# Kernel optimization log

Hardware: AMD Instinct MI355X
Metric: run time of the kernel (lower is better)

Reference implementation:

```python
import jax, jax.numpy as jnp
import numpy as np

B, N, E, D = 1, 50000, 800000, 128


def _mlp(x, w1, b1, w2, b2, w3, b3):
    # MLP(in, hidden, out, l=2): Linear+ReLU, Linear+ReLU, Linear
    h = jax.nn.relu(x @ w1 + b1)
    h = jax.nn.relu(h @ w2 + b2)
    return h @ w3 + b3


def _glorot(key, shape):
    fan_in, fan_out = shape[0], shape[1]
    lim = np.sqrt(6.0 / (fan_in + fan_out)).astype(np.float32)
    return jax.random.uniform(key, shape, jnp.float32, -lim, lim)


def setup_inputs() -> dict:
    key = jax.random.key(0)
    ks = jax.random.split(key, 16)
    inp = {
        "nodes": jax.random.normal(ks[0], (B, N, D), jnp.float32),
        "senders": jax.random.randint(ks[1], (E,), 0, N, jnp.int32),
        "receivers": jax.random.randint(ks[2], (E,), 0, N, jnp.int32),
        # message MLP params: 2D -> D -> D -> D
        "mw1": _glorot(ks[3], (2 * D, D)), "mb1": jnp.zeros((D,), jnp.float32),
        "mw2": _glorot(ks[4], (D, D)),     "mb2": jnp.zeros((D,), jnp.float32),
        "mw3": _glorot(ks[5], (D, D)),     "mb3": jnp.zeros((D,), jnp.float32),
        # node MLP params: 2D -> D -> D -> D
        "nw1": _glorot(ks[6], (2 * D, D)), "nb1": jnp.zeros((D,), jnp.float32),
        "nw2": _glorot(ks[7], (D, D)),     "nb2": jnp.zeros((D,), jnp.float32),
        "nw3": _glorot(ks[8], (D, D)),     "nb3": jnp.zeros((D,), jnp.float32),
    }
    return inp


def reference(nodes, senders, receivers,
              mw1, mb1, mw2, mb2, mw3, mb3,
              nw1, nb1, nw2, nb2, nw3, nb3):
    # gather endpoint features: [B, E, 2D]
    edge_in = jnp.concatenate((nodes[:, receivers], nodes[:, senders]), axis=-1)
    messages = _mlp(edge_in, mw1, mb1, mw2, mb2, mw3, mb3)  # [B, E, D]
    # scatter-add messages into receiver inbox: [B, N, D]
    inbox = jnp.zeros_like(nodes).at[:, receivers].add(messages)
    node_in = jnp.concatenate((nodes, inbox), axis=-1)  # [B, N, 2D]
    return nodes + _mlp(node_in, nw1, nb1, nw2, nb2, nw3, nb3)
```

## Files before the change

kernel.cpp:

```cpp
#include <hip/hip_runtime.h>
#include <hip/hip_bf16.h>
#include <stdint.h>

typedef __bf16 bf16;
typedef bf16 bf16x8 __attribute__((ext_vector_type(8)));
typedef float f32x4 __attribute__((ext_vector_type(4)));

#define N_NODES 50000
#define FEAT 128
#define NB_SCAN ((N_NODES + 1023) / 1024)

static constexpr size_t UV_BYTES    = (size_t)N_NODES * 256 * 2;
static constexpr size_t INBOX_BYTES = (size_t)N_NODES * FEAT * 4;

#define WUV_OFF 0
#define WM2_OFF 32768
#define WM3_OFF 49152
#define WN1_OFF 65536
#define WN2_OFF 98304
#define WN3_OFF 114688
#define W_TOTAL 131072
static constexpr size_t W_BYTES = (size_t)W_TOTAL * 2;

__device__ __forceinline__ bf16x8 cvt_f32x8_bf16(const float* __restrict__ p) {
  float4 f0 = *(const float4*)p;
  float4 f1 = *(const float4*)(p + 4);
  bf16x8 t;
  t[0] = (bf16)f0.x; t[1] = (bf16)f0.y; t[2] = (bf16)f0.z; t[3] = (bf16)f0.w;
  t[4] = (bf16)f1.x; t[5] = (bf16)f1.y; t[6] = (bf16)f1.z; t[7] = (bf16)f1.w;
  return t;
}

__global__ void prep_weights_kernel(const float* __restrict__ mw1, const float* __restrict__ mw2,
                                    const float* __restrict__ mw3, const float* __restrict__ nw1,
                                    const float* __restrict__ nw2, const float* __restrict__ nw3,
                                    bf16* __restrict__ w) {
  int i = blockIdx.x * blockDim.x + threadIdx.x;
  if (i >= W_TOTAL) return;
  float v;
  if (i < WM2_OFF) {
    int c = i >> 7, k = i & 127;
    v = (c < 128) ? mw1[k * 128 + c] : mw1[(128 + k) * 128 + (c - 128)];
  } else if (i < WM3_OFF) {
    int j = i - WM2_OFF; int c = j >> 7, k = j & 127;
    v = mw2[k * 128 + c];
  } else if (i < WN1_OFF) {
    int j = i - WM3_OFF; int c = j >> 7, k = j & 127;
    v = mw3[k * 128 + c];
  } else if (i < WN2_OFF) {
    int j = i - WN1_OFF; int c = j >> 8, k = j & 255;
    v = nw1[k * 128 + c];
  } else if (i < WN3_OFF) {
    int j = i - WN2_OFF; int c = j >> 7, k = j & 127;
    v = nw2[k * 128 + c];
  } else {
    int j = i - WN3_OFF; int c = j >> 7, k = j & 127;
    v = nw3[k * 128 + c];
  }
  w[i] = (bf16)v;
}

__global__ void hist_kernel(const int* __restrict__ receivers, int* __restrict__ cnt, int E) {
  int i = blockIdx.x * blockDim.x + threadIdx.x;
  if (i < E) atomicAdd(&cnt[receivers[i]], 1);
}

__global__ __launch_bounds__(1024) void scan1_kernel(const int* __restrict__ cnt,
                                                     int* __restrict__ offs,
                                                     int* __restrict__ bsum) {
  __shared__ int s[1024];
  const int tid = threadIdx.x;
  const int g = blockIdx.x * 1024 + tid;
  int x = (g < N_NODES) ? cnt[g] : 0;
  s[tid] = x;
  __syncthreads();
  for (int off = 1; off < 1024; off <<= 1) {
    int v = (tid >= off) ? s[tid - off] : 0;
    __syncthreads();
    s[tid] += v;
    __syncthreads();
  }
  if (g < N_NODES) offs[g] = s[tid] - x;
  if (tid == 1023) bsum[blockIdx.x] = s[tid];
}

__global__ void scan2_kernel(int* __restrict__ bsum) {
  __shared__ int s[64];
  const int tid = threadIdx.x;
  int x = (tid < NB_SCAN) ? bsum[tid] : 0;
  s[tid] = x;
  __syncthreads();
  for (int off = 1; off < 64; off <<= 1) {
    int v = (tid >= off) ? s[tid - off] : 0;
    __syncthreads();
    s[tid] += v;
    __syncthreads();
  }
  if (tid < NB_SCAN) bsum[tid] = s[tid] - x;
}

__global__ __launch_bounds__(1024) void scan3_kernel(int* __restrict__ offs,
                                                     const int* __restrict__ bsum, int E) {
  const int tid = threadIdx.x;
  const int g = blockIdx.x * 1024 + tid;
  if (g < N_NODES) offs[g] += bsum[blockIdx.x];
  if (blockIdx.x == 0 && tid == 0) offs[N_NODES] = E;
}

__global__ void pos_kernel(const int* __restrict__ receivers, const int* __restrict__ offs,
                           int* __restrict__ cur, int* __restrict__ pos, int E) {
  int i = blockIdx.x * blockDim.x + threadIdx.x;
  if (i < E) {
    int r = receivers[i];
    pos[i] = offs[r] + atomicAdd(&cur[r], 1);
  }
}

__global__ __launch_bounds__(512) void uv_gemm_kernel(const float* __restrict__ nodes,
                                                      const bf16* __restrict__ wuvt,
                                                      const float* __restrict__ mb1,
                                                      bf16* __restrict__ uv) {
  const int tid = threadIdx.x;
  const int lane = tid & 63, wid = tid >> 6;
  const int wm = wid >> 2, wn = wid & 3;
  const int rBase = blockIdx.x * 128 + wm * 64;
  const int cBase = wn * 64;
  const int l15 = lane & 15, ka = (lane >> 4) * 8, rj = (lane >> 4) * 4;

  f32x4 acc[4][4];
#pragma unroll
  for (int mi = 0; mi < 4; ++mi)
#pragma unroll
    for (int ni = 0; ni < 4; ++ni) acc[mi][ni] = (f32x4){0.f, 0.f, 0.f, 0.f};

#pragma unroll
  for (int kk = 0; kk < 4; ++kk) {
    const int k0 = kk * 32 + ka;
    bf16x8 a[4], b[4];
#pragma unroll
    for (int mi = 0; mi < 4; ++mi) {
      int r = rBase + mi * 16 + l15;
      if (r > N_NODES - 1) r = N_NODES - 1;
      a[mi] = cvt_f32x8_bf16(nodes + (size_t)r * FEAT + k0);
    }
#pragma unroll
    for (int ni = 0; ni < 4; ++ni) {
      int c = cBase + ni * 16 + l15;
      b[ni] = *(const bf16x8*)(wuvt + (size_t)c * 128 + k0);
    }
#pragma unroll
    for (int mi = 0; mi < 4; ++mi)
#pragma unroll
      for (int ni = 0; ni < 4; ++ni)
        acc[mi][ni] = __builtin_amdgcn_mfma_f32_16x16x32_bf16(a[mi], b[ni], acc[mi][ni], 0, 0, 0);
  }
#pragma unroll
  for (int mi = 0; mi < 4; ++mi)
#pragma unroll
    for (int ni = 0; ni < 4; ++ni) {
      int c = cBase + ni * 16 + l15;
      float bias = (c < FEAT) ? mb1[c] : 0.f;
#pragma unroll
      for (int j = 0; j < 4; ++j) {
        int r = rBase + mi * 16 + rj + j;
        if (r < N_NODES) uv[(size_t)r * 256 + c] = (bf16)(acc[mi][ni][j] + bias);
      }
    }
}

#define EB 128
template <bool SORT>
__global__ __launch_bounds__(256, 3) void edge_kernel(const bf16* __restrict__ uv,
                                                      const int* __restrict__ senders,
                                                      const int* __restrict__ receivers,
                                                      const int* __restrict__ pos,
                                                      const bf16* __restrict__ wm2t,
                                                      const bf16* __restrict__ wm3t,
                                                      const float* __restrict__ mb2,
                                                      const float* __restrict__ mb3,
                                                      bf16* __restrict__ msg,
                                                      float* __restrict__ inbox, int E) {
  __shared__ int rIds[EB];
  __shared__ int sIds[EB];
  __shared__ int pIds[EB];
  __shared__ bf16 hbuf[4][32 * 128];

  const int tid = threadIdx.x;
  const int e0 = blockIdx.x * EB;
  const int rMax = (E - e0 < EB) ? (E - e0) : EB;

  if (tid < EB) {
    int e = e0 + tid; if (e >= E) e = E - 1;
    rIds[tid] = receivers[e];
    if (SORT) pIds[tid] = pos[e];
  } else {
    int t = tid - EB;
    int e = e0 + t; if (e >= E) e = E - 1;
    sIds[t] = senders[e];
  }
  __syncthreads();

  const int lane = tid & 63, wid = tid >> 6;
  const int l15 = lane & 15, ka = (lane >> 4) * 8, rj = (lane >> 4) * 4;
  const int rW = wid * 32;
  bf16* hw = hbuf[wid];

  bf16x8 afr[2][4];
#pragma unroll
  for (int mi = 0; mi < 2; ++mi) {
    int row = rW + mi * 16 + l15;
    int recv = rIds[row], send = sIds[row];
    const bf16* up = uv + (size_t)recv * 256;
    const bf16* vp = uv + (size_t)send * 256 + 128;
#pragma unroll
    for (int kk = 0; kk < 4; ++kk) {
      int k0 = kk * 32 + ka;
      bf16x8 u8 = *(const bf16x8*)(up + k0);
      bf16x8 v8 = *(const bf16x8*)(vp + k0);
      bf16x8 h;
#pragma unroll
      for (int t = 0; t < 8; ++t) {
        float x = (float)u8[t] + (float)v8[t];
        h[t] = (bf16)(x > 0.f ? x : 0.f);
      }
      afr[mi][kk] = h;
    }
  }

  f32x4 acc[2][8];
#pragma unroll
  for (int mi = 0; mi < 2; ++mi)
#pragma unroll
    for (int ni = 0; ni < 8; ++ni) acc[mi][ni] = (f32x4){0.f, 0.f, 0.f, 0.f};
#pragma unroll
  for (int kk = 0; kk < 4; ++kk) {
    const int k0 = kk * 32 + ka;
    bf16x8 b[8];
#pragma unroll
    for (int ni = 0; ni < 8; ++ni) {
      int c = ni * 16 + l15;
      b[ni] = *(const bf16x8*)(wm2t + (size_t)c * 128 + k0);
    }
#pragma unroll
    for (int mi = 0; mi < 2; ++mi)
#pragma unroll
      for (int ni = 0; ni < 8; ++ni)
        acc[mi][ni] = __builtin_amdgcn_mfma_f32_16x16x32_bf16(afr[mi][kk], b[ni], acc[mi][ni], 0, 0, 0);
  }

#pragma unroll
  for (int mi = 0; mi < 2; ++mi)
#pragma unroll
    for (int ni = 0; ni < 8; ++ni) {
      int c = ni * 16 + l15;
      float bias = mb2[c];
#pragma unroll
      for (int j = 0; j < 4; ++j) {
        int row = mi * 16 + rj + j;
        float v = acc[mi][ni][j] + bias;
        v = v > 0.f ? v : 0.f;
        int byte = row * 256 + ((c * 2) ^ ((row & 7) << 4));
        *(bf16*)((char*)hw + byte) = (bf16)v;
      }
    }
  asm volatile("s_waitcnt lgkmcnt(0)" ::: "memory");
  __builtin_amdgcn_sched_barrier(0);

  bf16x8 a3[2][4];
#pragma unroll
  for (int mi = 0; mi < 2; ++mi) {
    int row = mi * 16 + l15;
#pragma unroll
    for (int kk = 0; kk < 4; ++kk) {
      int k0 = kk * 32 + ka;
      int byte = row * 256 + ((k0 * 2) ^ ((row & 7) << 4));
      a3[mi][kk] = *(const bf16x8*)((const char*)hw + byte);
    }
  }
  f32x4 acc3[2][8];
#pragma unroll
  for (int mi = 0; mi < 2; ++mi)
#pragma unroll
    for (int ni = 0; ni < 8; ++ni) acc3[mi][ni] = (f32x4){0.f, 0.f, 0.f, 0.f};
#pragma unroll
  for (int kk = 0; kk < 4; ++kk) {
    const int k0 = kk * 32 + ka;
    bf16x8 b[8];
#pragma unroll
    for (int ni = 0; ni < 8; ++ni) {
      int c = ni * 16 + l15;
      b[ni] = *(const bf16x8*)(wm3t + (size_t)c * 128 + k0);
    }
#pragma unroll
    for (int mi = 0; mi < 2; ++mi)
#pragma unroll
      for (int ni = 0; ni < 8; ++ni)
        acc3[mi][ni] = __builtin_amdgcn_mfma_f32_16x16x32_bf16(a3[mi][kk], b[ni], acc3[mi][ni], 0, 0, 0);
  }

  if (SORT) {
    asm volatile("s_waitcnt lgkmcnt(0)" ::: "memory");
    __builtin_amdgcn_sched_barrier(0);
#pragma unroll
    for (int mi = 0; mi < 2; ++mi)
#pragma unroll
      for (int ni = 0; ni < 8; ++ni) {
        int c = ni * 16 + l15;
        float bias = mb3[c];
#pragma unroll
        for (int j = 0; j < 4; ++j) {
          int row = mi * 16 + rj + j;
          int byte = row * 256 + ((c * 2) ^ ((row & 7) << 4));
          *(bf16*)((char*)hw + byte) = (bf16)(acc3[mi][ni][j] + bias);
        }
      }
    asm volatile("s_waitcnt lgkmcnt(0)" ::: "memory");
    __builtin_amdgcn_sched_barrier(0);
#pragma unroll
    for (int it = 0; it < 8; ++it) {
      int idx = it * 64 + lane;
      int row = idx >> 4, ch = idx & 15;
      int byte = row * 256 + ((ch * 16) ^ ((row & 7) << 4));
      bf16x8 m = *(const bf16x8*)((const char*)hw + byte);
      int grow = rW + row;
      if (grow < rMax)
        *(bf16x8*)(msg + (size_t)pIds[grow] * FEAT + ch * 8) = m;
    }
  } else {
#pragma unroll
    for (int mi = 0; mi < 2; ++mi)
#pragma unroll
      for (int ni = 0; ni < 8; ++ni) {
        int c = ni * 16 + l15;
        float bias = mb3[c];
#pragma unroll
        for (int j = 0; j < 4; ++j) {
          int row = rW + mi * 16 + rj + j;
          if (row < rMax)
            unsafeAtomicAdd(inbox + (size_t)rIds[row] * FEAT + c, acc3[mi][ni][j] + bias);
        }
      }
  }
}

__global__ __launch_bounds__(256) void reduce_kernel(const bf16* __restrict__ msg,
                                                     const int* __restrict__ offs,
                                                     float* __restrict__ inbox) {
  const int tid = threadIdx.x;
  const int n = blockIdx.x * 64 + (tid >> 2);
  if (n >= N_NODES) return;
  const int sub = tid & 3;
  const int beg = offs[n], end = offs[n + 1];

  float acc[4][8];
#pragma unroll
  for (int q = 0; q < 4; ++q)
#pragma unroll
    for (int t = 0; t < 8; ++t) acc[q][t] = 0.f;

  for (int j = beg; j < end; ++j) {
    const bf16* row = msg + (size_t)j * FEAT + sub * 32;
#pragma unroll
    for (int q = 0; q < 4; ++q) {
      bf16x8 m = *(const bf16x8*)(row + q * 8);
#pragma unroll
      for (int t = 0; t < 8; ++t) acc[q][t] += (float)m[t];
    }
  }
  float* dst = inbox + (size_t)n * FEAT + sub * 32;
#pragma unroll
  for (int q = 0; q < 4; ++q) {
    float4 v0 = {acc[q][0], acc[q][1], acc[q][2], acc[q][3]};
    float4 v1 = {acc[q][4], acc[q][5], acc[q][6], acc[q][7]};
    *(float4*)(dst + q * 8) = v0;
    *(float4*)(dst + q * 8 + 4) = v1;
  }
}

__global__ __launch_bounds__(512) void node_kernel(const float* __restrict__ nodes,
                                                   const float* __restrict__ inbox,
                                                   const bf16* __restrict__ wn1t,
                                                   const bf16* __restrict__ wn2t,
                                                   const bf16* __restrict__ wn3t,
                                                   const float* __restrict__ nb1,
                                                   const float* __restrict__ nb2,
                                                   const float* __restrict__ nb3,
                                                   float* __restrict__ out) {
  __shared__ bf16 h1[256 * 128];
  __shared__ bf16 h2[256 * 128];
  const int tid = threadIdx.x;
  const int lane = tid & 63, wid = tid >> 6;
  const int wm = wid >> 1, wn = wid & 1;
  const int rBase = wm * 64, cBase = wn * 64;
  const int l15 = lane & 15, ka = (lane >> 4) * 8, rj = (lane >> 4) * 4;
  const int nBase = blockIdx.x * 256;

  f32x4 acc[4][4];
#pragma unroll
  for (int mi = 0; mi < 4; ++mi)
#pragma unroll
    for (int ni = 0; ni < 4; ++ni) acc[mi][ni] = (f32x4){0.f, 0.f, 0.f, 0.f};
#pragma unroll
  for (int kk = 0; kk < 8; ++kk) {
    const int k0 = kk * 32 + ka;
    bf16x8 a[4], b[4];
#pragma unroll
    for (int mi = 0; mi < 4; ++mi) {
      int n = nBase + rBase + mi * 16 + l15;
      if (n > N_NODES - 1) n = N_NODES - 1;
      const float* src = (kk < 4) ? (nodes + (size_t)n * FEAT + k0)
                                  : (inbox + (size_t)n * FEAT + (k0 - 128));
      a[mi] = cvt_f32x8_bf16(src);
    }
#pragma unroll
    for (int ni = 0; ni < 4; ++ni) {
      int c = cBase + ni * 16 + l15;
      b[ni] = *(const bf16x8*)(wn1t + (size_t)c * 256 + k0);
    }
#pragma unroll
    for (int mi = 0; mi < 4; ++mi)
#pragma unroll
      for (int ni = 0; ni < 4; ++ni)
        acc[mi][ni] = __builtin_amdgcn_mfma_f32_16x16x32_bf16(a[mi], b[ni], acc[mi][ni], 0, 0, 0);
  }
#pragma unroll
  for (int mi = 0; mi < 4; ++mi)
#pragma unroll
    for (int ni = 0; ni < 4; ++ni) {
      int c = cBase + ni * 16 + l15;
      float bias = nb1[c];
#pragma unroll
      for (int j = 0; j < 4; ++j) {
        int r = rBase + mi * 16 + rj + j;
        float v = acc[mi][ni][j] + bias;
        v = v > 0.f ? v : 0.f;
        int byte = r * 256 + ((c * 2) ^ ((r & 7) << 4));
        *(bf16*)((char*)h1 + byte) = (bf16)v;
      }
    }
  __syncthreads();

#pragma unroll
  for (int mi = 0; mi < 4; ++mi)
#pragma unroll
    for (int ni = 0; ni < 4; ++ni) acc[mi][ni] = (f32x4){0.f, 0.f, 0.f, 0.f};
#pragma unroll
  for (int kk = 0; kk < 4; ++kk) {
    const int k0 = kk * 32 + ka;
    bf16x8 a[4], b[4];
#pragma unroll
    for (int mi = 0; mi < 4; ++mi) {
      int r = rBase + mi * 16 + l15;
      int byte = r * 256 + ((k0 * 2) ^ ((r & 7) << 4));
      a[mi] = *(const bf16x8*)((const char*)h1 + byte);
    }
#pragma unroll
    for (int ni = 0; ni < 4; ++ni) {
      int c = cBase + ni * 16 + l15;
      b[ni] = *(const bf16x8*)(wn2t + (size_t)c * 128 + k0);
    }
#pragma unroll
    for (int mi = 0; mi < 4; ++mi)
#pragma unroll
      for (int ni = 0; ni < 4; ++ni)
        acc[mi][ni] = __builtin_amdgcn_mfma_f32_16x16x32_bf16(a[mi], b[ni], acc[mi][ni], 0, 0, 0);
  }
#pragma unroll
  for (int mi = 0; mi < 4; ++mi)
#pragma unroll
    for (int ni = 0; ni < 4; ++ni) {
      int c = cBase + ni * 16 + l15;
      float bias = nb2[c];
#pragma unroll
      for (int j = 0; j < 4; ++j) {
        int r = rBase + mi * 16 + rj + j;
        float v = acc[mi][ni][j] + bias;
        v = v > 0.f ? v : 0.f;
        int byte = r * 256 + ((c * 2) ^ ((r & 7) << 4));
        *(bf16*)((char*)h2 + byte) = (bf16)v;
      }
    }
  __syncthreads();

#pragma unroll
  for (int mi = 0; mi < 4; ++mi)
#pragma unroll
    for (int ni = 0; ni < 4; ++ni) acc[mi][ni] = (f32x4){0.f, 0.f, 0.f, 0.f};
#pragma unroll
  for (int kk = 0; kk < 4; ++kk) {
    const int k0 = kk * 32 + ka;
    bf16x8 a[4], b[4];
#pragma unroll
    for (int mi = 0; mi < 4; ++mi) {
      int r = rBase + mi * 16 + l15;
      int byte = r * 256 + ((k0 * 2) ^ ((r & 7) << 4));
      a[mi] = *(const bf16x8*)((const char*)h2 + byte);
    }
#pragma unroll
    for (int ni = 0; ni < 4; ++ni) {
      int c = cBase + ni * 16 + l15;
      b[ni] = *(const bf16x8*)(wn3t + (size_t)c * 128 + k0);
    }
#pragma unroll
    for (int mi = 0; mi < 4; ++mi)
#pragma unroll
      for (int ni = 0; ni < 4; ++ni)
        acc[mi][ni] = __builtin_amdgcn_mfma_f32_16x16x32_bf16(a[mi], b[ni], acc[mi][ni], 0, 0, 0);
  }
#pragma unroll
  for (int mi = 0; mi < 4; ++mi)
#pragma unroll
    for (int ni = 0; ni < 4; ++ni) {
      int c = cBase + ni * 16 + l15;
      float bias = nb3[c];
#pragma unroll
      for (int j = 0; j < 4; ++j) {
        int r = rBase + mi * 16 + rj + j;
        int n = nBase + r;
        if (n < N_NODES)
          out[(size_t)n * FEAT + c] = nodes[(size_t)n * FEAT + c] + acc[mi][ni][j] + bias;
      }
    }
}

extern "C" void kernel_launch(void* const* d_in, const int* in_sizes, int n_in,
                              void* d_out, int out_size, void* d_ws, size_t ws_size,
                              hipStream_t stream) {
  const float* nodes = (const float*)d_in[0];
  const int* senders = (const int*)d_in[1];
  const int* receivers = (const int*)d_in[2];
  const float* mw1 = (const float*)d_in[3];
  const float* mb1 = (const float*)d_in[4];
  const float* mw2 = (const float*)d_in[5];
  const float* mb2 = (const float*)d_in[6];
  const float* mw3 = (const float*)d_in[7];
  const float* mb3 = (const float*)d_in[8];
  const float* nw1 = (const float*)d_in[9];
  const float* nb1 = (const float*)d_in[10];
  const float* nw2 = (const float*)d_in[11];
  const float* nb2 = (const float*)d_in[12];
  const float* nw3 = (const float*)d_in[13];
  const float* nb3 = (const float*)d_in[14];
  float* out = (float*)d_out;
  const int E = in_sizes[1];

  char* ws = (char*)d_ws;
  bf16* uv = (bf16*)ws;
  bf16* w = (bf16*)(ws + UV_BYTES);
  char* p = ws + UV_BYTES + W_BYTES;
  float* inbox = (float*)p; p += INBOX_BYTES;

  int* offs = (int*)p; p += ((size_t)(N_NODES + 1) * 4 + 255) & ~255ull;
  int* cnt = (int*)p;  p += ((size_t)N_NODES * 4 + 255) & ~255ull;
  int* cur = (int*)p;  p += ((size_t)N_NODES * 4 + 255) & ~255ull;
  int* pos = (int*)p;  p += ((size_t)E * 4 + 255) & ~255ull;
  bf16* msg = (bf16*)p; p += (size_t)E * FEAT * 2;
  const bool sortPath = ((size_t)(p - ws) <= ws_size);

  prep_weights_kernel<<<(W_TOTAL + 255) / 256, 256, 0, stream>>>(mw1, mw2, mw3, nw1, nw2, nw3, w);
  uv_gemm_kernel<<<(N_NODES + 127) / 128, 512, 0, stream>>>(nodes, w + WUV_OFF, mb1, uv);

  if (sortPath) {
    hipMemsetAsync(cnt, 0, (size_t)N_NODES * 4, stream);
    hipMemsetAsync(cur, 0, (size_t)N_NODES * 4, stream);
    hist_kernel<<<(E + 255) / 256, 256, 0, stream>>>(receivers, cnt, E);
    scan1_kernel<<<NB_SCAN, 1024, 0, stream>>>(cnt, offs, pos);
    scan2_kernel<<<1, 64, 0, stream>>>(pos);
    scan3_kernel<<<NB_SCAN, 1024, 0, stream>>>(offs, pos, E);
    pos_kernel<<<(E + 255) / 256, 256, 0, stream>>>(receivers, offs, cur, pos, E);
    edge_kernel<true><<<(E + EB - 1) / EB, 256, 0, stream>>>(uv, senders, receivers, pos,
                                                             w + WM2_OFF, w + WM3_OFF, mb2, mb3,
                                                             msg, inbox, E);
    reduce_kernel<<<(N_NODES + 63) / 64, 256, 0, stream>>>(msg, offs, inbox);
  } else {
    hipMemsetAsync(inbox, 0, INBOX_BYTES, stream);
    edge_kernel<false><<<(E + EB - 1) / EB, 256, 0, stream>>>(uv, senders, receivers, nullptr,
                                                              w + WM2_OFF, w + WM3_OFF, mb2, mb3,
                                                              nullptr, inbox, E);
  }
  node_kernel<<<(N_NODES + 255) / 256, 512, 0, stream>>>(nodes, inbox, w + WN1_OFF, w + WN2_OFF,
                                                         w + WN3_OFF, nb1, nb2, nb3, out);
}
```

Measured before the change: 501.7 us.

## Sort edges by receiver and segment-reduce messages in-block before atomics

Edges are now permuted into receiver-sorted order by scattering sender and receiver ids, so the edge kernel processes them in sorted order. Each warp transposes its message tile through LDS and accumulates runs of equal receivers in registers, issuing one atomic per run per column pair. This removes the per-edge bf16 message buffer write and the separate reduce kernel, trading them for atomics that are far fewer than per-edge ones. Gather locality on uv changes because sender access becomes more random while receiver access becomes sequential.

```diff
diff --git a/kernel.cpp b/kernel.cpp
--- a/kernel.cpp
+++ b/kernel.cpp
@@ -107,12 +107,16 @@
   if (blockIdx.x == 0 && tid == 0) offs[N_NODES] = E;
 }
 
-__global__ void pos_kernel(const int* __restrict__ receivers, const int* __restrict__ offs,
-                           int* __restrict__ cur, int* __restrict__ pos, int E) {
+__global__ void scatter_ids_kernel(const int* __restrict__ senders,
+                                   const int* __restrict__ receivers,
+                                   const int* __restrict__ offs, int* __restrict__ cur,
+                                   int* __restrict__ sSend, int* __restrict__ sRecv, int E) {
   int i = blockIdx.x * blockDim.x + threadIdx.x;
   if (i < E) {
     int r = receivers[i];
-    pos[i] = offs[r] + atomicAdd(&cur[r], 1);
+    int slot = offs[r] + atomicAdd(&cur[r], 1);
+    sSend[slot] = senders[i];
+    sRecv[slot] = r;
   }
 }
 
@@ -169,20 +173,16 @@
 }
 
 #define EB 128
-template <bool SORT>
 __global__ __launch_bounds__(256, 3) void edge_kernel(const bf16* __restrict__ uv,
-                                                      const int* __restrict__ senders,
-                                                      const int* __restrict__ receivers,
-                                                      const int* __restrict__ pos,
+                                                      const int* __restrict__ sSend,
+                                                      const int* __restrict__ sRecv,
                                                       const bf16* __restrict__ wm2t,
                                                       const bf16* __restrict__ wm3t,
                                                       const float* __restrict__ mb2,
                                                       const float* __restrict__ mb3,
-                                                      bf16* __restrict__ msg,
                                                       float* __restrict__ inbox, int E) {
   __shared__ int rIds[EB];
   __shared__ int sIds[EB];
-  __shared__ int pIds[EB];
   __shared__ bf16 hbuf[4][32 * 128];
 
   const int tid = threadIdx.x;
@@ -191,12 +191,11 @@
 
   if (tid < EB) {
     int e = e0 + tid; if (e >= E) e = E - 1;
-    rIds[tid] = receivers[e];
-    if (SORT) pIds[tid] = pos[e];
+    rIds[tid] = sRecv[e];
   } else {
     int t = tid - EB;
     int e = e0 + t; if (e >= E) e = E - 1;
-    sIds[t] = senders[e];
+    sIds[t] = sSend[e];
   }
   __syncthreads();
 
@@ -298,82 +297,46 @@
         acc3[mi][ni] = __builtin_amdgcn_mfma_f32_16x16x32_bf16(a3[mi][kk], b[ni], acc3[mi][ni], 0, 0, 0);
   }
 
-  if (SORT) {
-    asm volatile("s_waitcnt lgkmcnt(0)" ::: "memory");
-    __builtin_amdgcn_sched_barrier(0);
-#pragma unroll
-    for (int mi = 0; mi < 2; ++mi)
-#pragma unroll
-      for (int ni = 0; ni < 8; ++ni) {
-        int c = ni * 16 + l15;
-        float bias = mb3[c];
-#pragma unroll
-        for (int j = 0; j < 4; ++j) {
-          int row = mi * 16 + rj + j;
-          int byte = row * 256 + ((c * 2) ^ ((row & 7) << 4));
-          *(bf16*)((char*)hw + byte) = (bf16)(acc3[mi][ni][j] + bias);
-        }
-      }
-    asm volatile("s_waitcnt lgkmcnt(0)" ::: "memory");
-    __builtin_amdgcn_sched_barrier(0);
-#pragma unroll
-    for (int it = 0; it < 8; ++it) {
-      int idx = it * 64 + lane;
-      int row = idx >> 4, ch = idx & 15;
-      int byte = row * 256 + ((ch * 16) ^ ((row & 7) << 4));
-      bf16x8 m = *(const bf16x8*)((const char*)hw + byte);
-      int grow = rW + row;
-      if (grow < rMax)
-        *(bf16x8*)(msg + (size_t)pIds[grow] * FEAT + ch * 8) = m;
-    }
-  } else {
-#pragma unroll
-    for (int mi = 0; mi < 2; ++mi)
-#pragma unroll
-      for (int ni = 0; ni < 8; ++ni) {
-        int c = ni * 16 + l15;
-        float bias = mb3[c];
-#pragma unroll
-        for (int j = 0; j < 4; ++j) {
-          int row = rW + mi * 16 + rj + j;
-          if (row < rMax)
-            unsafeAtomicAdd(inbox + (size_t)rIds[row] * FEAT + c, acc3[mi][ni][j] + bias);
-        }
-      }
-  }
-}
-
-__global__ __launch_bounds__(256) void reduce_kernel(const bf16* __restrict__ msg,
-                                                     const int* __restrict__ offs,
-                                                     float* __restrict__ inbox) {
-  const int tid = threadIdx.x;
-  const int n = blockIdx.x * 64 + (tid >> 2);
-  if (n >= N_NODES) return;
-  const int sub = tid & 3;
-  const int beg = offs[n], end = offs[n + 1];
-
-  float acc[4][8];
-#pragma unroll
-  for (int q = 0; q < 4; ++q)
-#pragma unroll
-    for (int t = 0; t < 8; ++t) acc[q][t] = 0.f;
-
-  for (int j = beg; j < end; ++j) {
-    const bf16* row = msg + (size_t)j * FEAT + sub * 32;
-#pragma unroll
-    for (int q = 0; q < 4; ++q) {
-      bf16x8 m = *(const bf16x8*)(row + q * 8);
-#pragma unroll
-      for (int t = 0; t < 8; ++t) acc[q][t] += (float)m[t];
-    }
-  }
-  float* dst = inbox + (size_t)n * FEAT + sub * 32;
-#pragma unroll
-  for (int q = 0; q < 4; ++q) {
-    float4 v0 = {acc[q][0], acc[q][1], acc[q][2], acc[q][3]};
-    float4 v1 = {acc[q][4], acc[q][5], acc[q][6], acc[q][7]};
-    *(float4*)(dst + q * 8) = v0;
-    *(float4*)(dst + q * 8 + 4) = v1;
+  asm volatile("s_waitcnt lgkmcnt(0)" ::: "memory");
+  __builtin_amdgcn_sched_barrier(0);
+#pragma unroll
+  for (int mi = 0; mi < 2; ++mi)
+#pragma unroll
+    for (int ni = 0; ni < 8; ++ni) {
+      int c = ni * 16 + l15;
+      float bias = mb3[c];
+#pragma unroll
+      for (int j = 0; j < 4; ++j) {
+        int row = mi * 16 + rj + j;
+        int byte = row * 256 + ((c * 2) ^ ((row & 7) << 4));
+        *(bf16*)((char*)hw + byte) = (bf16)(acc3[mi][ni][j] + bias);
+      }
+    }
+  asm volatile("s_waitcnt lgkmcnt(0)" ::: "memory");
+  __builtin_amdgcn_sched_barrier(0);
+
+  uint32_t pr[32];
+#pragma unroll
+  for (int r = 0; r < 32; ++r) {
+    int byte = r * 256 + ((4 * lane) ^ ((r & 7) << 4));
+    pr[r] = *(const uint32_t*)((const char*)hw + byte);
+  }
+  const int cb = 2 * lane;
+  float s0 = 0.f, s1 = 0.f;
+#pragma unroll
+  for (int r = 0; r < 32; ++r) {
+    int grow = rW + r;
+    if (grow >= rMax) break;
+    s0 += __uint_as_float(pr[r] << 16);
+    s1 += __uint_as_float(pr[r] & 0xffff0000u);
+    int recv = rIds[grow];
+    bool flush = (r == 31) || (grow + 1 >= rMax) || (rIds[grow + 1] != recv);
+    if (flush) {
+      float* dst = inbox + (size_t)recv * FEAT + cb;
+      unsafeAtomicAdd(dst, s0);
+      unsafeAtomicAdd(dst + 1, s1);
+      s0 = 0.f; s1 = 0.f;
+    }
   }
 }
 
@@ -549,35 +512,26 @@
   bf16* w = (bf16*)(ws + UV_BYTES);
   char* p = ws + UV_BYTES + W_BYTES;
   float* inbox = (float*)p; p += INBOX_BYTES;
-
   int* offs = (int*)p; p += ((size_t)(N_NODES + 1) * 4 + 255) & ~255ull;
   int* cnt = (int*)p;  p += ((size_t)N_NODES * 4 + 255) & ~255ull;
   int* cur = (int*)p;  p += ((size_t)N_NODES * 4 + 255) & ~255ull;
-  int* pos = (int*)p;  p += ((size_t)E * 4 + 255) & ~255ull;
-  bf16* msg = (bf16*)p; p += (size_t)E * FEAT * 2;
-  const bool sortPath = ((size_t)(p - ws) <= ws_size);
-
+  int* bsum = (int*)p; p += 256;
+  int* sSend = (int*)p; p += ((size_t)E * 4 + 255) & ~255ull;
+  int* sRecv = (int*)p; p += ((size_t)E * 4 + 255) & ~255ull;
+
+  hipMemsetAsync(cnt, 0, (size_t)N_NODES * 4, stream);
+  hipMemsetAsync(cur, 0, (size_t)N_NODES * 4, stream);
+  hipMemsetAsync(inbox, 0, INBOX_BYTES, stream);
   prep_weights_kernel<<<(W_TOTAL + 255) / 256, 256, 0, stream>>>(mw1, mw2, mw3, nw1, nw2, nw3, w);
+  hist_kernel<<<(E + 255) / 256, 256, 0, stream>>>(receivers, cnt, E);
+  scan1_kernel<<<NB_SCAN, 1024, 0, stream>>>(cnt, offs, bsum);
+  scan2_kernel<<<1, 64, 0, stream>>>(bsum);
+  scan3_kernel<<<NB_SCAN, 1024, 0, stream>>>(offs, bsum, E);
+  scatter_ids_kernel<<<(E + 255) / 256, 256, 0, stream>>>(senders, receivers, offs, cur,
+                                                          sSend, sRecv, E);
   uv_gemm_kernel<<<(N_NODES + 127) / 128, 512, 0, stream>>>(nodes, w + WUV_OFF, mb1, uv);
-
-  if (sortPath) {
-    hipMemsetAsync(cnt, 0, (size_t)N_NODES * 4, stream);
-    hipMemsetAsync(cur, 0, (size_t)N_NODES * 4, stream);
-    hist_kernel<<<(E + 255) / 256, 256, 0, stream>>>(receivers, cnt, E);
-    scan1_kernel<<<NB_SCAN, 1024, 0, stream>>>(cnt, offs, pos);
-    scan2_kernel<<<1, 64, 0, stream>>>(pos);
-    scan3_kernel<<<NB_SCAN, 1024, 0, stream>>>(offs, pos, E);
-    pos_kernel<<<(E + 255) / 256, 256, 0, stream>>>(receivers, offs, cur, pos, E);
-    edge_kernel<true><<<(E + EB - 1) / EB, 256, 0, stream>>>(uv, senders, receivers, pos,
-                                                             w + WM2_OFF, w + WM3_OFF, mb2, mb3,
-                                                             msg, inbox, E);
-    reduce_kernel<<<(N_NODES + 63) / 64, 256, 0, stream>>>(msg, offs, inbox);
-  } else {
-    hipMemsetAsync(inbox, 0, INBOX_BYTES, stream);
-    edge_kernel<false><<<(E + EB - 1) / EB, 256, 0, stream>>>(uv, senders, receivers, nullptr,
-                                                              w + WM2_OFF, w + WM3_OFF, mb2, mb3,
-                                                              nullptr, inbox, E);
-  }
+  edge_kernel<<<(E + EB - 1) / EB, 256, 0, stream>>>(uv, sSend, sRecv, w + WM2_OFF, w + WM3_OFF,
+                                                     mb2, mb3, inbox, E);
   node_kernel<<<(N_NODES + 255) / 256, 512, 0, stream>>>(nodes, inbox, w + WN1_OFF, w + WN2_OFF,
                                                          w + WN3_OFF, nb1, nb2, nb3, out);
 }
```

Result: faster. 476.9 us (-4.9%).
